# Optimization experiments

Measured on AMD Instinct MI355X. Metric: run time of the kernel, lower is better.

## Reference

```python
import jax, jax.numpy as jnp
import numpy as np

B, N, D, OUT = 4, 512, 128, 128

def setup_inputs() -> dict:
    key = jax.random.key(0)
    k1, k2, k3, k4 = jax.random.split(key, 4)
    x = jax.random.normal(k1, (B, N, D), dtype=jnp.float32)
    # binary adjacency mask (float, as it multiplies edge features in the original)
    adj = (jax.random.uniform(k2, (B, N, N)) < 0.5).astype(jnp.float32)
    # nn.Linear(2D, OUT): store as (2D, OUT) so y = feat @ W + b
    W = jax.random.normal(k3, (2 * D, OUT), dtype=jnp.float32) * (1.0 / np.sqrt(2 * D))
    b = jax.random.normal(k4, (OUT,), dtype=jnp.float32) * 0.01
    return {"x": x, "adj": adj, "W": W, "b": b}

def reference(x, adj, W, b):
    # edge_feat = cat([x_i, x_j - x_i]); linear on concat decomposes as
    # x_i @ W1 + (x_j - x_i) @ W2 = x_i @ (W1 - W2) + x_j @ W2  -> avoids the (B,N,N,2D) concat.
    d = x.shape[-1]
    W1, W2 = W[:d], W[d:]
    p = jnp.einsum('bnd,do->bno', x, W1 - W2)   # contribution of x_i
    q = jnp.einsum('bnd,do->bno', x, W2)        # contribution of x_j
    pre = p[:, :, None, :] + q[:, None, :, :] + b  # (B, N, N, OUT)
    h = jax.nn.relu(pre) * adj[..., None]          # dropout is identity in eval mode
    return jnp.max(h, axis=2)                      # max over neighbors j -> (B, N, OUT)
```

## Files before the change

### kernel.cpp

```cpp
#include <hip/hip_runtime.h>

#define B_ 4
#define N_ 512
#define D_ 128
#define O_ 128

#define R1 8

__global__ __launch_bounds__(1024)
void gemm_pq_kernel(const float* __restrict__ x, const float* __restrict__ W,
                    const float* __restrict__ bias, float* __restrict__ q,
                    float* __restrict__ phat) {
    const int tid = threadIdx.x;
    const int o   = tid & (O_ - 1);
    const int kq  = __builtin_amdgcn_readfirstlane(tid >> 7);
    const int row0 = blockIdx.x * R1;

    const float* __restrict__ xb = x + (size_t)row0 * D_;

    float accp[R1], accq[R1];
#pragma unroll
    for (int r = 0; r < R1; ++r) { accp[r] = 0.0f; accq[r] = 0.0f; }

    const int k0 = kq * (D_ / 8);
#pragma unroll 4
    for (int k = k0; k < k0 + D_ / 8; ++k) {
        const float w1 = W[(size_t)k * O_ + o];
        const float w2 = W[(size_t)(k + D_) * O_ + o];
        const float wd = w1 - w2;
#pragma unroll
        for (int r = 0; r < R1; ++r) {
            const float xv = xb[(size_t)r * D_ + k];
            accp[r] = fmaf(xv, wd, accp[r]);
            accq[r] = fmaf(xv, w2, accq[r]);
        }
    }

    __shared__ float redq[R1][O_][9];
    __shared__ float redp[R1][O_][9];

#pragma unroll
    for (int r = 0; r < R1; ++r) {
        redq[r][o][kq] = accq[r];
        redp[r][o][kq] = accp[r];
    }
    __syncthreads();

    {
        const int rr = tid >> 7;
        const int oo = tid & (O_ - 1);
        const float sq = ((redq[rr][oo][0] + redq[rr][oo][1]) +
                          (redq[rr][oo][2] + redq[rr][oo][3])) +
                         ((redq[rr][oo][4] + redq[rr][oo][5]) +
                          (redq[rr][oo][6] + redq[rr][oo][7]));
        const float sp = ((redp[rr][oo][0] + redp[rr][oo][1]) +
                          (redp[rr][oo][2] + redp[rr][oo][3])) +
                         ((redp[rr][oo][4] + redp[rr][oo][5]) +
                          (redp[rr][oo][6] + redp[rr][oo][7]));
        const size_t idx = (size_t)(row0 + rr) * O_ + oo;
        q[idx]    = sq;
        phat[idx] = sp + bias[oo];
    }
}

#define TI 8
#define JS 8
#define JB 16

__global__ __launch_bounds__(1024)
void maskmax_kernel(const float* __restrict__ q, const float* __restrict__ phat,
                    const float* __restrict__ adj, float* __restrict__ out) {
    const int tid = threadIdx.x;
    const int o   = tid & (O_ - 1);
    const int jq  = __builtin_amdgcn_readfirstlane(tid >> 7);
    const int b   = blockIdx.x >> 6;
    const int i0  = (blockIdx.x & 63) * TI;

    const float* __restrict__ qb   = q + (size_t)b * N_ * O_ + o;
    const float* __restrict__ arow = adj + ((size_t)b * N_ + i0) * N_;

    float m[TI];
#pragma unroll
    for (int i = 0; i < TI; ++i) m[i] = -1e30f;

    const int j0   = jq * (N_ / JS);
    const int jend = j0 + (N_ / JS);

    float qv[JB], qn[JB];
#pragma unroll
    for (int u = 0; u < JB; ++u)
        qv[u] = qb[(size_t)(j0 + u) * O_];

    for (int j = j0; j < jend; j += JB) {
        const int jn = (j + JB < jend) ? (j + JB) : j0;
#pragma unroll
        for (int u = 0; u < JB; ++u)
            qn[u] = qb[(size_t)(jn + u) * O_];

#pragma unroll
        for (int i = 0; i < TI; ++i) {
            const float* __restrict__ ar = arow + (size_t)i * N_ + j;
            float c[JB];
#pragma unroll
            for (int u = 0; u < JB; ++u)
                c[u] = fmaf(ar[u], 1024.0f, qv[u]);
            float mi = m[i];
#pragma unroll
            for (int u = 0; u < JB; u += 4) {
                mi = fmaxf(mi, fmaxf(c[u],     c[u + 1]));
                mi = fmaxf(mi, fmaxf(c[u + 2], c[u + 3]));
            }
            m[i] = mi;
        }

#pragma unroll
        for (int u = 0; u < JB; ++u) qv[u] = qn[u];
    }

    __shared__ float part[TI][O_][JS + 1];
#pragma unroll
    for (int i = 0; i < TI; ++i) part[i][o][jq] = m[i];
    __syncthreads();

    {
        const int i  = tid >> 7;
        const int oo = tid & (O_ - 1);
        float mm = -1e30f;
#pragma unroll
        for (int p = 0; p < JS; ++p) mm = fmaxf(mm, part[i][oo][p]);
        const size_t idx = ((size_t)b * N_ + i0 + i) * O_ + oo;
        const float v = phat[idx] + mm - 1024.0f;
        out[idx] = v > 0.0f ? v : 0.0f;
    }
}

extern "C" void kernel_launch(void* const* d_in, const int* in_sizes, int n_in,
                              void* d_out, int out_size, void* d_ws, size_t ws_size,
                              hipStream_t stream) {
    const float* x    = (const float*)d_in[0];
    const float* adj  = (const float*)d_in[1];
    const float* W    = (const float*)d_in[2];
    const float* bias = (const float*)d_in[3];
    float* out = (float*)d_out;

    float* q    = (float*)d_ws;
    float* phat = q + (size_t)B_ * N_ * O_;

    gemm_pq_kernel<<<(B_ * N_) / R1, 1024, 0, stream>>>(x, W, bias, q, phat);
    maskmax_kernel<<<B_ * (N_ / TI), 1024, 0, stream>>>(q, phat, adj, out);
}
```

Baseline: 73.17 us.

## Retile maskmax over output halves with wider i-tiles and full register q slice

Each block of the mask-max kernel now covers 16 rows i and half of the output columns (64), with 16 j-splits of 32 neighbours each. Each thread loads all 32 of its q values into registers once, replacing the double-buffered streaming loop. The aim is to reuse q across more rows and cut loop overhead while keeping the same number of blocks. In exchange, adj rows are re-read by both output-half blocks, and register pressure rises.

```diff
diff --git a/kernel.cpp b/kernel.cpp
--- a/kernel.cpp
+++ b/kernel.cpp
@@ -63,72 +63,64 @@
     }
 }
 
-#define TI 8
-#define JS 8
-#define JB 16
+#define TI2 16
+#define JSP 16
 
 __global__ __launch_bounds__(1024)
 void maskmax_kernel(const float* __restrict__ q, const float* __restrict__ phat,
                     const float* __restrict__ adj, float* __restrict__ out) {
     const int tid = threadIdx.x;
-    const int o   = tid & (O_ - 1);
-    const int jq  = __builtin_amdgcn_readfirstlane(tid >> 7);
-    const int b   = blockIdx.x >> 6;
-    const int i0  = (blockIdx.x & 63) * TI;
+    const int o   = tid & 63;
+    const int jq  = __builtin_amdgcn_readfirstlane(tid >> 6);
+    const int blk = blockIdx.x;
+    const int b   = blk >> 6;
+    const int rem = blk & 63;
+    const int i0  = (rem >> 1) * TI2;
+    const int oh  = rem & 1;
+    const int ocol = oh * 64 + o;
 
-    const float* __restrict__ qb   = q + (size_t)b * N_ * O_ + o;
+    const float* __restrict__ qb   = q + (size_t)b * N_ * O_ + ocol;
     const float* __restrict__ arow = adj + ((size_t)b * N_ + i0) * N_;
 
-    float m[TI];
+    const int j0 = jq * (N_ / JSP);
+
+    float qv[32];
 #pragma unroll
-    for (int i = 0; i < TI; ++i) m[i] = -1e30f;
-
-    const int j0   = jq * (N_ / JS);
-    const int jend = j0 + (N_ / JS);
-
-    float qv[JB], qn[JB];
-#pragma unroll
-    for (int u = 0; u < JB; ++u)
+    for (int u = 0; u < 32; ++u)
         qv[u] = qb[(size_t)(j0 + u) * O_];
 
-    for (int j = j0; j < jend; j += JB) {
-        const int jn = (j + JB < jend) ? (j + JB) : j0;
+    float m[TI2];
 #pragma unroll
-        for (int u = 0; u < JB; ++u)
-            qn[u] = qb[(size_t)(jn + u) * O_];
+    for (int i = 0; i < TI2; ++i) m[i] = -1e30f;
 
 #pragma unroll
-        for (int i = 0; i < TI; ++i) {
-            const float* __restrict__ ar = arow + (size_t)i * N_ + j;
-            float c[JB];
+    for (int i = 0; i < TI2; ++i) {
+        const float* __restrict__ ar = arow + (size_t)i * N_ + j0;
+        float c[32];
 #pragma unroll
-            for (int u = 0; u < JB; ++u)
-                c[u] = fmaf(ar[u], 1024.0f, qv[u]);
-            float mi = m[i];
+        for (int u = 0; u < 32; ++u)
+            c[u] = fmaf(ar[u], 1024.0f, qv[u]);
+        float mi = m[i];
 #pragma unroll
-            for (int u = 0; u < JB; u += 4) {
-                mi = fmaxf(mi, fmaxf(c[u],     c[u + 1]));
-                mi = fmaxf(mi, fmaxf(c[u + 2], c[u + 3]));
-            }
-            m[i] = mi;
+        for (int u = 0; u < 32; u += 4) {
+            mi = fmaxf(mi, fmaxf(c[u],     c[u + 1]));
+            mi = fmaxf(mi, fmaxf(c[u + 2], c[u + 3]));
         }
-
-#pragma unroll
-        for (int u = 0; u < JB; ++u) qv[u] = qn[u];
+        m[i] = mi;
     }
 
-    __shared__ float part[TI][O_][JS + 1];
+    __shared__ float part[TI2][64][JSP + 1];
 #pragma unroll
-    for (int i = 0; i < TI; ++i) part[i][o][jq] = m[i];
+    for (int i = 0; i < TI2; ++i) part[i][o][jq] = m[i];
     __syncthreads();
 
     {
-        const int i  = tid >> 7;
-        const int oo = tid & (O_ - 1);
+        const int ii = tid >> 6;
+        const int oo = tid & 63;
         float mm = -1e30f;
 #pragma unroll
-        for (int p = 0; p < JS; ++p) mm = fmaxf(mm, part[i][oo][p]);
-        const size_t idx = ((size_t)b * N_ + i0 + i) * O_ + oo;
+        for (int p = 0; p < JSP; ++p) mm = fmaxf(mm, part[ii][oo][p]);
+        const size_t idx = ((size_t)b * N_ + i0 + ii) * O_ + (oh * 64 + oo);
         const float v = phat[idx] + mm - 1024.0f;
         out[idx] = v > 0.0f ? v : 0.0f;
     }
@@ -147,5 +139,5 @@
     float* phat = q + (size_t)B_ * N_ * O_;
 
     gemm_pq_kernel<<<(B_ * N_) / R1, 1024, 0, stream>>>(x, W, bias, q, phat);
-    maskmax_kernel<<<B_ * (N_ / TI), 1024, 0, stream>>>(q, phat, adj, out);
+    maskmax_kernel<<<B_ * 64, 1024, 0, stream>>>(q, phat, adj, out);
 }
```

Result: slower. 76.74 us (+4.9%).
